# Kernel tuning notes

Measured on AMD Instinct MI355X. Metric: run time of the kernel, lower is better.

## Reference

```python
import jax, jax.numpy as jnp
import numpy as np
import math

B, L, IN, OUT = 32, 2048, 182, 2
H, N2, NL = 256, 32, 4  # hidden_dim, d_state//2, num_layers


def setup_inputs() -> dict:
    key = jax.random.key(0)
    ks = jax.random.split(key, 12)
    neural_input = jax.random.normal(ks[0], (B, L, IN), jnp.float32)
    # input / output projections
    Win = jax.random.normal(ks[1], (IN, H), jnp.float32) / np.sqrt(IN)
    b_in = jnp.zeros((H,), jnp.float32)
    Wout = jax.random.normal(ks[2], (H, OUT), jnp.float32) / np.sqrt(H)
    b_out = jnp.zeros((OUT,), jnp.float32)
    # stacked per-layer S4D params
    C2 = jax.random.normal(ks[3], (NL, H, N2, 2), jnp.float32)  # view_as_real of complex C
    log_dt = jax.random.uniform(ks[4], (NL, H), jnp.float32) * (math.log(0.1) - math.log(0.001)) + math.log(0.001)
    log_A_real = jnp.full((NL, H, N2), math.log(0.5), jnp.float32)
    A_imag = math.pi * jnp.broadcast_to(jnp.arange(N2, dtype=jnp.float32), (NL, H, N2))
    D = jax.random.normal(ks[5], (NL, H), jnp.float32)
    Wglu = jax.random.normal(ks[6], (NL, 2 * H, H), jnp.float32) / np.sqrt(H)
    bglu = jnp.zeros((NL, 2 * H), jnp.float32)
    return {"neural_input": neural_input, "Win": Win, "b_in": b_in,
            "C2": C2, "log_dt": log_dt, "log_A_real": log_A_real, "A_imag": A_imag,
            "D": D, "Wglu": Wglu, "bglu": bglu, "Wout": Wout, "b_out": b_out}


def _s4d_kernel(C2, log_dt, log_A_real, A_imag, length):
    # dt: (H,), A: (H,N2) complex
    dt = jnp.exp(log_dt)
    A = -jnp.exp(log_A_real) + 1j * A_imag
    dtA = A * dt[:, None]                      # (H, N2)
    C = (C2[..., 0] + 1j * C2[..., 1]) * (jnp.exp(dtA) - 1.0) / A
    t = jnp.arange(length, dtype=jnp.float32)
    E = jnp.exp(dtA[..., None] * t)            # (H, N2, L) complex
    K = 2.0 * jnp.einsum('hn,hnl->hl', C, E).real  # (H, L)
    return K


def _s4d_layer(u, C2, log_dt, log_A_real, A_imag, D, Wg, bg):
    # u: (B, H, L)
    length = u.shape[-1]
    k = _s4d_kernel(C2, log_dt, log_A_real, A_imag, length)
    k_f = jnp.fft.rfft(k, n=2 * length)        # (H, L+1)
    u_f = jnp.fft.rfft(u, n=2 * length)        # (B, H, L+1)
    y = jnp.fft.irfft(u_f * k_f, n=2 * length)[..., :length]
    y = y + u * D[:, None]
    y = jax.nn.gelu(y, approximate=False)      # nn.GELU default (erf)
    z = jnp.einsum('oh,bhl->bol', Wg, y) + bg[None, :, None]  # Conv1d k=1
    a, g = jnp.split(z, 2, axis=1)             # GLU over channel dim
    return a * jax.nn.sigmoid(g)


def reference(neural_input, Win, b_in, C2, log_dt, log_A_real, A_imag, D, Wglu, bglu, Wout, b_out):
    # input projection: (B, L, IN) -> (B, H, L)
    x = (neural_input @ Win + b_in).transpose(0, 2, 1)
    for i in range(NL):
        x = _s4d_layer(x, C2[i], log_dt[i], log_A_real[i], A_imag[i], D[i], Wglu[i], bglu[i])
    x = x.transpose(0, 2, 1)                   # (B, L, H)
    return x @ Wout + b_out                    # (B, L, OUT)
```

## Files before the change

### kernel.cpp

```cpp
#include <hip/hip_runtime.h>
#include <math.h>

typedef unsigned short u16;
typedef __attribute__((ext_vector_type(2))) unsigned short ushort2_t;
typedef __attribute__((ext_vector_type(4))) unsigned short ushort4_t;
typedef __attribute__((ext_vector_type(8))) unsigned short ushort8_t;
typedef __attribute__((ext_vector_type(8))) short short8;
typedef __attribute__((ext_vector_type(4))) float f32x4;

constexpr int Bn = 32, Ln = 2048, IN_DIM = 182, OUT_DIM = 2;
constexpr int Hn = 256, N2n = 32, NLn = 4;
constexpr int Tn = 64, NCn = Ln / Tn;
constexpr int KP = 192;

__device__ inline u16 f2bf(float f) {
  unsigned int u = __float_as_uint(f);
  u += 0x7fffu + ((u >> 16) & 1u);
  return (u16)(u >> 16);
}
__device__ inline float bf2f(u16 v) { return __uint_as_float(((unsigned int)v) << 16); }

__global__ void k_consts(const float* __restrict__ C2, const float* __restrict__ log_dt,
                         const float* __restrict__ log_A_real, const float* __restrict__ A_imag,
                         float* __restrict__ cAT, float* __restrict__ cC, float* __restrict__ cDt) {
  int idx = blockIdx.x * blockDim.x + threadIdx.x;
  if (idx >= NLn * Hn * N2n) return;
  int lh = idx / N2n;
  int h = lh % Hn;
  int l = lh / Hn;
  float dt = expf(log_dt[l * Hn + h]);
  float Ar = -expf(log_A_real[idx]);
  float Ai = A_imag[idx];
  float dr = Ar * dt, di = Ai * dt;
  float ea = expf(dr);
  float ar = ea * cosf(di), ai = ea * sinf(di);
  float eT = expf(dr * (float)Tn);
  cAT[idx * 2 + 0] = eT * cosf(di * (float)Tn);
  cAT[idx * 2 + 1] = eT * sinf(di * (float)Tn);
  float nr = ar - 1.0f, ni = ai;
  float inv = 1.0f / (Ar * Ar + Ai * Ai);
  float qr = (nr * Ar + ni * Ai) * inv;
  float qi = (ni * Ar - nr * Ai) * inv;
  float c2r = C2[idx * 2 + 0], c2i = C2[idx * 2 + 1];
  cC[idx * 2 + 0] = 2.0f * (c2r * qr - c2i * qi);
  cC[idx * 2 + 1] = 2.0f * (c2r * qi + c2i * qr);
  cDt[idx * 2 + 0] = dr;
  cDt[idx * 2 + 1] = di;
}

__global__ __launch_bounds__(256) void k_ktab(const float* __restrict__ cDt,
                                              const float* __restrict__ cC,
                                              float* __restrict__ ktab) {
  __shared__ float tmp[32][65];
  __shared__ float part[4][64];
  int lh = blockIdx.x;
  int tid = threadIdx.x;
  int n = tid >> 3, dq = tid & 7;
  float dr = cDt[(lh * N2n + n) * 2 + 0], di = cDt[(lh * N2n + n) * 2 + 1];
  float Cr = cC[(lh * N2n + n) * 2 + 0], Ci = cC[(lh * N2n + n) * 2 + 1];
  float d0 = (float)(dq * 8);
  float e0 = expf(dr * d0);
  float pr = e0 * cosf(di * d0), pi = e0 * sinf(di * d0);
  float ea = expf(dr);
  float ar = ea * cosf(di), ai = ea * sinf(di);
#pragma unroll
  for (int j = 0; j < 8; j++) {
    tmp[n][dq * 8 + j] = Cr * pr - Ci * pi;
    float t = pr * ar - pi * ai;
    pi = pr * ai + pi * ar;
    pr = t;
  }
  __syncthreads();
  int d = tid & 63, q = tid >> 6;
  float s = 0.0f;
#pragma unroll
  for (int k = 0; k < 8; k++) s += tmp[q * 8 + k][d];
  part[q][d] = s;
  __syncthreads();
  if (tid < 64) ktab[lh * 64 + tid] = part[0][tid] + part[1][tid] + part[2][tid] + part[3][tid];
}

__global__ void k_build(const float* __restrict__ cDt, const float* __restrict__ cC,
                        const float* __restrict__ ktab, const float* __restrict__ Dp,
                        u16* __restrict__ Lm, u16* __restrict__ Em, u16* __restrict__ Fm) {
  int h = blockIdx.x;
  int ym = blockIdx.y;
  int l = ym / 3, mat = ym % 3;
  int tid = threadIdx.x;
  int lh = l * Hn + h;
  if (mat == 2) {
    int n2 = tid & 31, tg = tid >> 5;
    float dr = cDt[(lh * N2n + n2) * 2 + 0], di = cDt[(lh * N2n + n2) * 2 + 1];
    float Cr = cC[(lh * N2n + n2) * 2 + 0], Ci = cC[(lh * N2n + n2) * 2 + 1];
    float p0 = (float)(tg * 8 + 1);
    float e0 = expf(dr * p0);
    float pr = e0 * cosf(di * p0), pi = e0 * sinf(di * p0);
    float ea = expf(dr);
    float ar = ea * cosf(di), ai = ea * sinf(di);
#pragma unroll
    for (int j = 0; j < 8; j++) {
      float wr = Cr * pr - Ci * pi;
      float wi = Cr * pi + Ci * pr;
      ushort2_t o; o[0] = f2bf(wr); o[1] = f2bf(-wi);
      *(ushort2_t*)(Fm + (size_t)lh * 4096 + (tg * 8 + j) * 64 + n2 * 2) = o;
      float t = pr * ar - pi * ai;
      pi = pr * ai + pi * ar;
      pr = t;
    }
    return;
  }
  int row = tid >> 2, tq = (tid & 3) * 16;
  u16 vals[16];
  if (mat == 0) {
    float Dh = Dp[lh];
    for (int j = 0; j < 16; j++) {
      int tau = tq + j;
      int d = row - tau;
      float v = 0.0f;
      if (d >= 0) { v = ktab[lh * 64 + d]; if (d == 0) v += Dh; }
      vals[j] = f2bf(v);
    }
  } else {
    int n = row >> 1, im = row & 1;
    float dr = cDt[(lh * N2n + n) * 2 + 0], di = cDt[(lh * N2n + n) * 2 + 1];
    float p0 = (float)(48 - tq);
    float e0 = expf(dr * p0);
    float pr = e0 * cosf(di * p0), pi = e0 * sinf(di * p0);
    float ea = expf(dr);
    float ar = ea * cosf(di), ai = ea * sinf(di);
#pragma unroll
    for (int j = 15; j >= 0; j--) {
      vals[j] = f2bf(im ? pi : pr);
      float t = pr * ar - pi * ai;
      pi = pr * ai + pi * ar;
      pr = t;
    }
  }
  u16* dst = (mat == 0 ? Lm : Em) + (size_t)lh * 4096 + row * 64 + tq;
  ushort8_t o0, o1;
  for (int j = 0; j < 8; j++) { o0[j] = vals[j]; o1[j] = vals[8 + j]; }
  *(ushort8_t*)dst = o0;
  *(ushort8_t*)(dst + 8) = o1;
}

__global__ void k_wf(const float* __restrict__ Wglu, u16* __restrict__ Wf) {
  int idx = blockIdx.x * blockDim.x + threadIdx.x;
  if (idx >= NLn * 2 * Hn * Hn) return;
  int k = idx & 255;
  int o = (idx >> 8) & 511;
  int l = idx >> 17;
  size_t off = (size_t)l * (32 * 8192) + (size_t)(o >> 4) * 8192
             + (size_t)(k >> 3) * 256 + (o & 15) * 16 + (k & 7) * 2;
  *(u16*)((char*)Wf + off) = f2bf(Wglu[idx]);
}

__global__ void k_wtin(const float* __restrict__ Win, u16* __restrict__ Wt) {
  int idx = blockIdx.x * blockDim.x + threadIdx.x;
  if (idx >= Hn * KP) return;
  int h = idx / KP, k = idx - h * KP;
  Wt[idx] = (k < IN_DIM) ? f2bf(Win[(size_t)k * Hn + h]) : (u16)0;
}

__global__ __launch_bounds__(256) void k_inproj(const float* __restrict__ nin,
                                                const u16* __restrict__ Wt,
                                                const float* __restrict__ b_in,
                                                u16* __restrict__ Xc) {
  int tid = threadIdx.x;
  int bx = blockIdx.x;
  int nb = blockIdx.y;
  int lane = tid & 63, wave = tid >> 6;
  int wm = wave >> 1, wn = wave & 1;
  int l15 = lane & 15, l4 = lane >> 4;
  int m0 = bx * 128 + wm * 64;
  int h0 = nb * 128 + wn * 64;
  f32x4 acc[4][4] = {};
#pragma unroll
  for (int ks = 0; ks < 6; ks++) {
    int k0 = ks * 32 + l4 * 8;
    short8 a[4], bfr[4];
#pragma unroll
    for (int mt = 0; mt < 4; mt++) {
      const float* rp = nin + (size_t)(m0 + mt * 16 + l15) * IN_DIM + k0;
      short8 v;
      if (k0 + 8 <= IN_DIM) {
        float2 f0 = *(const float2*)(rp);
        float2 f1 = *(const float2*)(rp + 2);
        float2 f2 = *(const float2*)(rp + 4);
        float2 f3 = *(const float2*)(rp + 6);
        v[0] = (short)f2bf(f0.x); v[1] = (short)f2bf(f0.y);
        v[2] = (short)f2bf(f1.x); v[3] = (short)f2bf(f1.y);
        v[4] = (short)f2bf(f2.x); v[5] = (short)f2bf(f2.y);
        v[6] = (short)f2bf(f3.x); v[7] = (short)f2bf(f3.y);
      } else {
#pragma unroll
        for (int j = 0; j < 8; j++) {
          int k = k0 + j;
          float x = (k < IN_DIM) ? rp[j] : 0.0f;
          v[j] = (short)f2bf(x);
        }
      }
      a[mt] = v;
    }
#pragma unroll
    for (int nt = 0; nt < 4; nt++)
      bfr[nt] = *(const short8*)(Wt + (size_t)(h0 + nt * 16 + l15) * KP + k0);
#pragma unroll
    for (int mt = 0; mt < 4; mt++)
#pragma unroll
      for (int nt = 0; nt < 4; nt++)
        acc[mt][nt] = __builtin_amdgcn_mfma_f32_16x16x32_bf16(a[mt], bfr[nt], acc[mt][nt], 0, 0, 0);
  }
#pragma unroll
  for (int mt = 0; mt < 4; mt++) {
#pragma unroll
    for (int nt = 0; nt < 4; nt++) {
      int j = h0 + nt * 16 + l15;
      float bb = b_in[j];
      int r0 = m0 + mt * 16 + l4 * 4;
      int b = r0 >> 11, li = r0 & 2047;
      int c = li >> 6, t0 = li & 63;
      ushort4_t w;
#pragma unroll
      for (int r = 0; r < 4; r++) w[r] = f2bf(acc[mt][nt][r] + bb);
      *(ushort4_t*)(Xc + ((size_t)(b * NCn + c) * Hn + j) * Tn + t0) = w;
    }
  }
}

__global__ __launch_bounds__(512, 6) void k_s4d(const u16* __restrict__ Xc,
                                                const u16* __restrict__ Lm,
                                                const u16* __restrict__ Em,
                                                const u16* __restrict__ Fm,
                                                const float* __restrict__ cAT,
                                                u16* __restrict__ Gf, int layer) {
  __shared__ __align__(16) char sbuf[32768];
  __shared__ __align__(16) char ybuf[16384];
  int tid = threadIdx.x;
  int lane = tid & 63, w = tid >> 6;
  int l15 = lane & 15, l4 = lane >> 4;
  int hg = blockIdx.x;
  int b = blockIdx.y;
  int h = hg * 8 + w;

  short8 ufr[2][2];
  const u16* xb = Xc + ((size_t)(b * NCn) * Hn + h) * Tn;
#pragma unroll
  for (int nt = 0; nt < 2; nt++)
#pragma unroll
    for (int ks = 0; ks < 2; ks++)
      ufr[nt][ks] = *(const short8*)(xb + (size_t)(nt * 16 + l15) * (Hn * Tn) + ks * 32 + l4 * 8);
  const u16* eb = Em + (size_t)(layer * Hn + h) * 4096;
#pragma unroll
  for (int mt = 0; mt < 4; mt++) {
    f32x4 sacc[2] = {};
#pragma unroll
    for (int ks = 0; ks < 2; ks++) {
      short8 af = *(const short8*)(eb + (mt * 16 + l15) * 64 + ks * 32 + l4 * 8);
#pragma unroll
      for (int nt = 0; nt < 2; nt++)
        sacc[nt] = __builtin_amdgcn_mfma_f32_16x16x32_bf16(af, ufr[nt][ks], sacc[nt], 0, 0, 0);
    }
    int comp0 = mt * 16 + l4 * 4;
    int g = comp0 >> 3, half = (comp0 >> 2) & 1;
#pragma unroll
    for (int nt = 0; nt < 2; nt++) {
      int c = nt * 16 + l15;
      ushort4_t wv;
#pragma unroll
      for (int r = 0; r < 4; r++) wv[r] = f2bf(sacc[nt][r]);
      *(ushort4_t*)(sbuf + w * 4096 + c * 128 + ((g ^ (c & 7)) << 4) + half * 8) = wv;
    }
  }
  __syncthreads();
  if (tid < 256) {
    int hl = tid >> 5, n = tid & 31;
    int hh = hg * 8 + hl;
    float aTr = cAT[((size_t)(layer * Hn + hh) * N2n + n) * 2 + 0];
    float aTi = cAT[((size_t)(layer * Hn + hh) * N2n + n) * 2 + 1];
    int grp = n >> 2, off = (n & 3) * 4;
    char* base = sbuf + hl * 4096;
    float cr = 0.0f, ci = 0.0f;
#pragma unroll
    for (int p = 0; p < 4; p++) {
      unsigned int sv[8];
#pragma unroll
      for (int q = 0; q < 8; q++) {
        int c = p * 8 + q;
        sv[q] = *(const unsigned int*)(base + c * 128 + ((grp ^ (c & 7)) << 4) + off);
      }
#pragma unroll
      for (int q = 0; q < 8; q++) {
        unsigned int s = sv[q];
        float sre = bf2f((u16)(s & 0xffffu));
        float sim = bf2f((u16)(s >> 16));
        sv[q] = (unsigned int)f2bf(cr) | ((unsigned int)f2bf(ci) << 16);
        float nr = aTr * cr - aTi * ci + sre;
        float ni = aTr * ci + aTi * cr + sim;
        cr = nr; ci = ni;
      }
#pragma unroll
      for (int q = 0; q < 8; q++) {
        int c = p * 8 + q;
        *(unsigned int*)(base + c * 128 + ((grp ^ (c & 7)) << 4) + off) = sv[q];
      }
    }
  }
  __syncthreads();
  const u16* lb = Lm + (size_t)(layer * Hn + h) * 4096;
  const u16* fb = Fm + (size_t)(layer * Hn + h) * 4096;
  u16* gp = Gf + (size_t)(hg * Bn + b) * Ln * 8;
  for (int nt = 0; nt < 2; nt++) {
    int c = nt * 16 + l15;
#pragma unroll
    for (int mt = 0; mt < 4; mt++) {
      f32x4 yacc = {};
#pragma unroll
      for (int ks = 0; ks < 2; ks++) {
        short8 af = *(const short8*)(lb + (mt * 16 + l15) * 64 + ks * 32 + l4 * 8);
        yacc = __builtin_amdgcn_mfma_f32_16x16x32_bf16(af, ufr[nt][ks], yacc, 0, 0, 0);
      }
#pragma unroll
      for (int ks = 0; ks < 2; ks++) {
        short8 af = *(const short8*)(fb + (mt * 16 + l15) * 64 + ks * 32 + l4 * 8);
        short8 bf = *(const short8*)(sbuf + w * 4096 + c * 128 + (((ks * 4 + l4) ^ (c & 7)) << 4));
        yacc = __builtin_amdgcn_mfma_f32_16x16x32_bf16(af, bf, yacc, 0, 0, 0);
      }
      int t0 = mt * 16 + l4 * 4;
      ushort4_t wv;
#pragma unroll
      for (int r = 0; r < 4; r++) {
        float y = yacc[r];
        wv[r] = f2bf(0.5f * y * (1.0f + erff(y * 0.70710678118654752f)));
      }
      int g = ((t0 >> 2) ^ l15) & 15;
      *(ushort4_t*)(ybuf + (l15 * 8 + w) * 128 + g * 8) = wv;
    }
    __syncthreads();
#pragma unroll
    for (int it = 0; it < 2; it++) {
      int mloc = it * 512 + tid;
      int cl = mloc >> 6, t = mloc & 63;
      int g = ((t >> 2) ^ cl) & 15;
      const char* bb = ybuf + (cl * 8) * 128 + g * 8 + (t & 3) * 2;
      ushort8_t o;
#pragma unroll
      for (int hl = 0; hl < 8; hl++) o[hl] = *(const u16*)(bb + hl * 128);
      int m = (nt * 16 + cl) * 64 + t;
      *(ushort8_t*)(gp + (size_t)m * 8) = o;
    }
    __syncthreads();
  }
}

template <int LAST>
__global__ __launch_bounds__(256) void k_glu(const u16* __restrict__ Gf,
                                             const u16* __restrict__ Wf,
                                             const float* __restrict__ bglu,
                                             u16* __restrict__ Xout, int layer) {
  int tid = threadIdx.x;
  int bx = blockIdx.x;
  int nb = blockIdx.y;
  int lane = tid & 63, wave = tid >> 6;
  int wm = wave >> 1, wn = wave & 1;
  int l15 = lane & 15, l4 = lane >> 4;
  int m0 = bx * 128 + wm * 64;
  const char* wb = (const char*)Wf + (size_t)layer * 262144 + lane * 16;
  f32x4 acc[4][4] = {};
#pragma unroll 2
  for (int ks = 0; ks < 8; ks++) {
    short8 a[4], bfr[4];
#pragma unroll
    for (int rg = 0; rg < 4; rg++)
      a[rg] = *(const short8*)(Gf + (size_t)(ks * 4 + l4) * 524288 + (size_t)(m0 + rg * 16 + l15) * 8);
#pragma unroll
    for (int ct = 0; ct < 2; ct++) {
      bfr[ct]     = *(const short8*)(wb + (size_t)(nb * 4 + wn * 2 + ct) * 8192 + ks * 1024);
      bfr[ct + 2] = *(const short8*)(wb + (size_t)(16 + nb * 4 + wn * 2 + ct) * 8192 + ks * 1024);
    }
#pragma unroll
    for (int rg = 0; rg < 4; rg++)
#pragma unroll
      for (int ct = 0; ct < 4; ct++)
        acc[rg][ct] = __builtin_amdgcn_mfma_f32_16x16x32_bf16(a[rg], bfr[ct], acc[rg][ct], 0, 0, 0);
  }
  int c0 = nb * 64 + wn * 32;
#pragma unroll
  for (int rg = 0; rg < 4; rg++) {
#pragma unroll
    for (int ct = 0; ct < 2; ct++) {
      int j = c0 + ct * 16 + l15;
      float ba = bglu[layer * 512 + j];
      float bg = bglu[layer * 512 + 256 + j];
      f32x4 va = acc[rg][ct], vg = acc[rg][ct + 2];
      int r0 = m0 + rg * 16 + l4 * 4;
      if (LAST) {
#pragma unroll
        for (int r = 0; r < 4; r++) {
          float za = va[r] + ba, zg = vg[r] + bg;
          Xout[(size_t)(r0 + r) * Hn + j] = f2bf(za / (1.0f + expf(-zg)));
        }
      } else {
        int b = r0 >> 11, li = r0 & 2047;
        int c = li >> 6, t0 = li & 63;
        ushort4_t w;
#pragma unroll
        for (int r = 0; r < 4; r++) {
          float za = va[r] + ba, zg = vg[r] + bg;
          w[r] = f2bf(za / (1.0f + expf(-zg)));
        }
        *(ushort4_t*)(Xout + ((size_t)(b * NCn + c) * Hn + j) * Tn + t0) = w;
      }
    }
  }
}

__global__ __launch_bounds__(256) void k_outproj(const u16* __restrict__ Xp,
                                                 const float* __restrict__ Wout,
                                                 const float* __restrict__ b_out,
                                                 float* __restrict__ out) {
  int row = blockIdx.x * 4 + (threadIdx.x >> 6);
  int lane = threadIdx.x & 63;
  ushort4_t xv = *(const ushort4_t*)(Xp + (size_t)row * Hn + lane * 4);
  float x0 = bf2f(xv[0]), x1 = bf2f(xv[1]), x2 = bf2f(xv[2]), x3 = bf2f(xv[3]);
  const float4 w01 = *(const float4*)&Wout[lane * 8];
  const float4 w23 = *(const float4*)&Wout[lane * 8 + 4];
  float p0 = x0 * w01.x + x1 * w01.z + x2 * w23.x + x3 * w23.z;
  float p1 = x0 * w01.y + x1 * w01.w + x2 * w23.y + x3 * w23.w;
  for (int off = 32; off; off >>= 1) {
    p0 += __shfl_down(p0, off, 64);
    p1 += __shfl_down(p1, off, 64);
  }
  if (lane == 0) {
    out[(size_t)row * 2 + 0] = p0 + b_out[0];
    out[(size_t)row * 2 + 1] = p1 + b_out[1];
  }
}

extern "C" void kernel_launch(void* const* d_in, const int* in_sizes, int n_in,
                              void* d_out, int out_size, void* d_ws, size_t ws_size,
                              hipStream_t stream) {
  const float* nin        = (const float*)d_in[0];
  const float* Win        = (const float*)d_in[1];
  const float* b_in       = (const float*)d_in[2];
  const float* C2         = (const float*)d_in[3];
  const float* log_dt     = (const float*)d_in[4];
  const float* log_A_real = (const float*)d_in[5];
  const float* A_imag     = (const float*)d_in[6];
  const float* Dp         = (const float*)d_in[7];
  const float* Wglu       = (const float*)d_in[8];
  const float* bglu       = (const float*)d_in[9];
  const float* Wout       = (const float*)d_in[10];
  const float* b_out      = (const float*)d_in[11];
  float* out = (float*)d_out;

  u16* Xc = (u16*)d_ws;
  u16* Gf = Xc + (size_t)16777216;
  u16* Wt = Gf + (size_t)16777216;
  u16* Wf = Wt + (size_t)49152;
  u16* Lm = Wf + (size_t)524288;
  u16* Em = Lm + (size_t)4194304;
  u16* Fm = Em + (size_t)4194304;
  float* ktab = (float*)(Fm + (size_t)4194304);
  float* cAT  = ktab + 65536;
  float* cC   = cAT + 65536;
  float* cDt  = cC + 65536;

  k_consts<<<(NLn * Hn * N2n + 255) / 256, 256, 0, stream>>>(C2, log_dt, log_A_real, A_imag, cAT, cC, cDt);
  k_ktab<<<NLn * Hn, 256, 0, stream>>>(cDt, cC, ktab);
  k_build<<<dim3(Hn, NLn * 3), 256, 0, stream>>>(cDt, cC, ktab, Dp, Lm, Em, Fm);
  k_wf<<<(NLn * 2 * Hn * Hn + 255) / 256, 256, 0, stream>>>(Wglu, Wf);
  k_wtin<<<(Hn * KP + 255) / 256, 256, 0, stream>>>(Win, Wt);
  k_inproj<<<dim3(512, 2), 256, 0, stream>>>(nin, Wt, b_in, Xc);
  for (int l = 0; l < NLn; l++) {
    k_s4d<<<dim3(32, Bn), 512, 0, stream>>>(Xc, Lm, Em, Fm, cAT, Gf, l);
    if (l < NLn - 1)
      k_glu<0><<<dim3(512, 4), 256, 0, stream>>>(Gf, Wf, bglu, Xc, l);
    else
      k_glu<1><<<dim3(512, 4), 256, 0, stream>>>(Gf, Wf, bglu, Xc, l);
  }
  k_outproj<<<Bn * Ln / 4, 256, 0, stream>>>(Xc, Wout, b_out, out);
}
```

Before: 518.4 us.

## Fuse S4D prep kernels, stage input tile in LDS, remap block order

Three setup kernels (consts, ktab, build) are merged into one per-(layer,h) kernel that holds the intermediate constants in shared memory, which removes two launches and the global round-trips for ktab/cC/cDt. The input projection now loads its 128-row fp32 tile coalesced into padded LDS as bf16 before the MFMA loop, instead of doing strided per-lane float2 loads. The s4d and glu launches switch to 1D grids with a swizzled block-to-tile mapping so that consecutive blocks are spread across the XCDs, meant to improve cache locality. The inproj kernel uses about 51KB of LDS, which may lower its occupancy.

```diff
diff --git a/kernel.cpp b/kernel.cpp
--- a/kernel.cpp
+++ b/kernel.cpp
@@ -12,6 +12,7 @@
 constexpr int Hn = 256, N2n = 32, NLn = 4;
 constexpr int Tn = 64, NCn = Ln / Tn;
 constexpr int KP = 192;
+constexpr int IPPAD = 200;
 
 __device__ inline u16 f2bf(float f) {
   unsigned int u = __float_as_uint(f);
@@ -20,78 +21,111 @@
 }
 __device__ inline float bf2f(u16 v) { return __uint_as_float(((unsigned int)v) << 16); }
 
-__global__ void k_consts(const float* __restrict__ C2, const float* __restrict__ log_dt,
-                         const float* __restrict__ log_A_real, const float* __restrict__ A_imag,
-                         float* __restrict__ cAT, float* __restrict__ cC, float* __restrict__ cDt) {
-  int idx = blockIdx.x * blockDim.x + threadIdx.x;
-  if (idx >= NLn * Hn * N2n) return;
-  int lh = idx / N2n;
-  int h = lh % Hn;
-  int l = lh / Hn;
-  float dt = expf(log_dt[l * Hn + h]);
-  float Ar = -expf(log_A_real[idx]);
-  float Ai = A_imag[idx];
-  float dr = Ar * dt, di = Ai * dt;
-  float ea = expf(dr);
-  float ar = ea * cosf(di), ai = ea * sinf(di);
-  float eT = expf(dr * (float)Tn);
-  cAT[idx * 2 + 0] = eT * cosf(di * (float)Tn);
-  cAT[idx * 2 + 1] = eT * sinf(di * (float)Tn);
-  float nr = ar - 1.0f, ni = ai;
-  float inv = 1.0f / (Ar * Ar + Ai * Ai);
-  float qr = (nr * Ar + ni * Ai) * inv;
-  float qi = (ni * Ar - nr * Ai) * inv;
-  float c2r = C2[idx * 2 + 0], c2i = C2[idx * 2 + 1];
-  cC[idx * 2 + 0] = 2.0f * (c2r * qr - c2i * qi);
-  cC[idx * 2 + 1] = 2.0f * (c2r * qi + c2i * qr);
-  cDt[idx * 2 + 0] = dr;
-  cDt[idx * 2 + 1] = di;
-}
-
-__global__ __launch_bounds__(256) void k_ktab(const float* __restrict__ cDt,
-                                              const float* __restrict__ cC,
-                                              float* __restrict__ ktab) {
+__global__ __launch_bounds__(256) void k_prep(const float* __restrict__ C2,
+                                              const float* __restrict__ log_dt,
+                                              const float* __restrict__ log_A_real,
+                                              const float* __restrict__ A_imag,
+                                              const float* __restrict__ Dp,
+                                              float* __restrict__ cAT,
+                                              u16* __restrict__ Lm, u16* __restrict__ Em,
+                                              u16* __restrict__ Fm) {
+  __shared__ float sdr[32], sdi[32], sCr[32], sCi[32];
   __shared__ float tmp[32][65];
   __shared__ float part[4][64];
+  __shared__ float kt[64];
   int lh = blockIdx.x;
   int tid = threadIdx.x;
-  int n = tid >> 3, dq = tid & 7;
-  float dr = cDt[(lh * N2n + n) * 2 + 0], di = cDt[(lh * N2n + n) * 2 + 1];
-  float Cr = cC[(lh * N2n + n) * 2 + 0], Ci = cC[(lh * N2n + n) * 2 + 1];
-  float d0 = (float)(dq * 8);
-  float e0 = expf(dr * d0);
-  float pr = e0 * cosf(di * d0), pi = e0 * sinf(di * d0);
-  float ea = expf(dr);
-  float ar = ea * cosf(di), ai = ea * sinf(di);
-#pragma unroll
-  for (int j = 0; j < 8; j++) {
-    tmp[n][dq * 8 + j] = Cr * pr - Ci * pi;
-    float t = pr * ar - pi * ai;
-    pi = pr * ai + pi * ar;
-    pr = t;
-  }
-  __syncthreads();
-  int d = tid & 63, q = tid >> 6;
-  float s = 0.0f;
-#pragma unroll
-  for (int k = 0; k < 8; k++) s += tmp[q * 8 + k][d];
-  part[q][d] = s;
-  __syncthreads();
-  if (tid < 64) ktab[lh * 64 + tid] = part[0][tid] + part[1][tid] + part[2][tid] + part[3][tid];
-}
-
-__global__ void k_build(const float* __restrict__ cDt, const float* __restrict__ cC,
-                        const float* __restrict__ ktab, const float* __restrict__ Dp,
-                        u16* __restrict__ Lm, u16* __restrict__ Em, u16* __restrict__ Fm) {
-  int h = blockIdx.x;
-  int ym = blockIdx.y;
-  int l = ym / 3, mat = ym % 3;
-  int tid = threadIdx.x;
-  int lh = l * Hn + h;
-  if (mat == 2) {
+  if (tid < 32) {
+    int n = tid;
+    int idx = lh * N2n + n;
+    float dt = expf(log_dt[lh]);
+    float Ar = -expf(log_A_real[idx]);
+    float Ai = A_imag[idx];
+    float dr = Ar * dt, di = Ai * dt;
+    float ea = expf(dr);
+    float ar = ea * cosf(di), ai = ea * sinf(di);
+    float eT = expf(dr * 64.0f);
+    cAT[idx * 2 + 0] = eT * cosf(di * 64.0f);
+    cAT[idx * 2 + 1] = eT * sinf(di * 64.0f);
+    float nr = ar - 1.0f, ni = ai;
+    float inv = 1.0f / (Ar * Ar + Ai * Ai);
+    float qr = (nr * Ar + ni * Ai) * inv;
+    float qi = (ni * Ar - nr * Ai) * inv;
+    float c2r = C2[idx * 2 + 0], c2i = C2[idx * 2 + 1];
+    sdr[n] = dr; sdi[n] = di;
+    sCr[n] = 2.0f * (c2r * qr - c2i * qi);
+    sCi[n] = 2.0f * (c2r * qi + c2i * qr);
+  }
+  __syncthreads();
+  {
+    int n = tid >> 3, dq = tid & 7;
+    float dr = sdr[n], di = sdi[n], Cr = sCr[n], Ci = sCi[n];
+    float d0 = (float)(dq * 8);
+    float e0 = expf(dr * d0);
+    float pr = e0 * cosf(di * d0), pi = e0 * sinf(di * d0);
+    float ea = expf(dr);
+    float ar = ea * cosf(di), ai = ea * sinf(di);
+#pragma unroll
+    for (int j = 0; j < 8; j++) {
+      tmp[n][dq * 8 + j] = Cr * pr - Ci * pi;
+      float t = pr * ar - pi * ai;
+      pi = pr * ai + pi * ar;
+      pr = t;
+    }
+  }
+  __syncthreads();
+  {
+    int d = tid & 63, q = tid >> 6;
+    float s = 0.0f;
+#pragma unroll
+    for (int k = 0; k < 8; k++) s += tmp[q * 8 + k][d];
+    part[q][d] = s;
+  }
+  __syncthreads();
+  if (tid < 64) kt[tid] = part[0][tid] + part[1][tid] + part[2][tid] + part[3][tid];
+  __syncthreads();
+  {
+    int row = tid >> 2, tq = (tid & 3) * 16;
+    float Dh = Dp[lh];
+    u16 vals[16];
+    for (int j = 0; j < 16; j++) {
+      int d = row - (tq + j);
+      float v = 0.0f;
+      if (d >= 0) { v = kt[d]; if (d == 0) v += Dh; }
+      vals[j] = f2bf(v);
+    }
+    u16* dst = Lm + (size_t)lh * 4096 + row * 64 + tq;
+    ushort8_t o0, o1;
+    for (int j = 0; j < 8; j++) { o0[j] = vals[j]; o1[j] = vals[8 + j]; }
+    *(ushort8_t*)dst = o0;
+    *(ushort8_t*)(dst + 8) = o1;
+  }
+  {
+    int row = tid >> 2, tq = (tid & 3) * 16;
+    int n = row >> 1, im = row & 1;
+    float dr = sdr[n], di = sdi[n];
+    float p0 = (float)(48 - tq);
+    float e0 = expf(dr * p0);
+    float pr = e0 * cosf(di * p0), pi = e0 * sinf(di * p0);
+    float ea = expf(dr);
+    float ar = ea * cosf(di), ai = ea * sinf(di);
+    u16 vals[16];
+#pragma unroll
+    for (int j = 15; j >= 0; j--) {
+      vals[j] = f2bf(im ? pi : pr);
+      float t = pr * ar - pi * ai;
+      pi = pr * ai + pi * ar;
+      pr = t;
+    }
+    u16* dst = Em + (size_t)lh * 4096 + row * 64 + tq;
+    ushort8_t o0, o1;
+    for (int j = 0; j < 8; j++) { o0[j] = vals[j]; o1[j] = vals[8 + j]; }
+    *(ushort8_t*)dst = o0;
+    *(ushort8_t*)(dst + 8) = o1;
+  }
+  {
     int n2 = tid & 31, tg = tid >> 5;
-    float dr = cDt[(lh * N2n + n2) * 2 + 0], di = cDt[(lh * N2n + n2) * 2 + 1];
-    float Cr = cC[(lh * N2n + n2) * 2 + 0], Ci = cC[(lh * N2n + n2) * 2 + 1];
+    float dr = sdr[n2], di = sdi[n2], Cr = sCr[n2], Ci = sCi[n2];
     float p0 = (float)(tg * 8 + 1);
     float e0 = expf(dr * p0);
     float pr = e0 * cosf(di * p0), pi = e0 * sinf(di * p0);
@@ -107,40 +141,7 @@
       pi = pr * ai + pi * ar;
       pr = t;
     }
-    return;
-  }
-  int row = tid >> 2, tq = (tid & 3) * 16;
-  u16 vals[16];
-  if (mat == 0) {
-    float Dh = Dp[lh];
-    for (int j = 0; j < 16; j++) {
-      int tau = tq + j;
-      int d = row - tau;
-      float v = 0.0f;
-      if (d >= 0) { v = ktab[lh * 64 + d]; if (d == 0) v += Dh; }
-      vals[j] = f2bf(v);
-    }
-  } else {
-    int n = row >> 1, im = row & 1;
-    float dr = cDt[(lh * N2n + n) * 2 + 0], di = cDt[(lh * N2n + n) * 2 + 1];
-    float p0 = (float)(48 - tq);
-    float e0 = expf(dr * p0);
-    float pr = e0 * cosf(di * p0), pi = e0 * sinf(di * p0);
-    float ea = expf(dr);
-    float ar = ea * cosf(di), ai = ea * sinf(di);
-#pragma unroll
-    for (int j = 15; j >= 0; j--) {
-      vals[j] = f2bf(im ? pi : pr);
-      float t = pr * ar - pi * ai;
-      pi = pr * ai + pi * ar;
-      pr = t;
-    }
-  }
-  u16* dst = (mat == 0 ? Lm : Em) + (size_t)lh * 4096 + row * 64 + tq;
-  ushort8_t o0, o1;
-  for (int j = 0; j < 8; j++) { o0[j] = vals[j]; o1[j] = vals[8 + j]; }
-  *(ushort8_t*)dst = o0;
-  *(ushort8_t*)(dst + 8) = o1;
+  }
 }
 
 __global__ void k_wf(const float* __restrict__ Wglu, u16* __restrict__ Wf) {
@@ -165,13 +166,33 @@
                                                 const u16* __restrict__ Wt,
                                                 const float* __restrict__ b_in,
                                                 u16* __restrict__ Xc) {
+  __shared__ __align__(16) u16 at[128 * IPPAD];
   int tid = threadIdx.x;
   int bx = blockIdx.x;
   int nb = blockIdx.y;
+  int m0 = bx * 128;
+  for (int i = tid; i < 128 * (IPPAD - IN_DIM); i += 256) {
+    int r = i / (IPPAD - IN_DIM), c = IN_DIM + i - r * (IPPAD - IN_DIM);
+    at[r * IPPAD + c] = 0;
+  }
+  const float4* src = (const float4*)(nin + (size_t)m0 * IN_DIM);
+  for (int i = tid; i < 128 * IN_DIM / 4; i += 256) {
+    float4 v = src[i];
+    int e0 = i * 4;
+    int r = e0 / IN_DIM;
+    int c = e0 - r * IN_DIM;
+    float vv[4] = {v.x, v.y, v.z, v.w};
+#pragma unroll
+    for (int j = 0; j < 4; j++) {
+      int rr = r, cc = c + j;
+      if (cc >= IN_DIM) { rr++; cc -= IN_DIM; }
+      at[rr * IPPAD + cc] = f2bf(vv[j]);
+    }
+  }
+  __syncthreads();
   int lane = tid & 63, wave = tid >> 6;
   int wm = wave >> 1, wn = wave & 1;
   int l15 = lane & 15, l4 = lane >> 4;
-  int m0 = bx * 128 + wm * 64;
   int h0 = nb * 128 + wn * 64;
   f32x4 acc[4][4] = {};
 #pragma unroll
@@ -179,28 +200,8 @@
     int k0 = ks * 32 + l4 * 8;
     short8 a[4], bfr[4];
 #pragma unroll
-    for (int mt = 0; mt < 4; mt++) {
-      const float* rp = nin + (size_t)(m0 + mt * 16 + l15) * IN_DIM + k0;
-      short8 v;
-      if (k0 + 8 <= IN_DIM) {
-        float2 f0 = *(const float2*)(rp);
-        float2 f1 = *(const float2*)(rp + 2);
-        float2 f2 = *(const float2*)(rp + 4);
-        float2 f3 = *(const float2*)(rp + 6);
-        v[0] = (short)f2bf(f0.x); v[1] = (short)f2bf(f0.y);
-        v[2] = (short)f2bf(f1.x); v[3] = (short)f2bf(f1.y);
-        v[4] = (short)f2bf(f2.x); v[5] = (short)f2bf(f2.y);
-        v[6] = (short)f2bf(f3.x); v[7] = (short)f2bf(f3.y);
-      } else {
-#pragma unroll
-        for (int j = 0; j < 8; j++) {
-          int k = k0 + j;
-          float x = (k < IN_DIM) ? rp[j] : 0.0f;
-          v[j] = (short)f2bf(x);
-        }
-      }
-      a[mt] = v;
-    }
+    for (int mt = 0; mt < 4; mt++)
+      a[mt] = *(const short8*)&at[(wm * 64 + mt * 16 + l15) * IPPAD + k0];
 #pragma unroll
     for (int nt = 0; nt < 4; nt++)
       bfr[nt] = *(const short8*)(Wt + (size_t)(h0 + nt * 16 + l15) * KP + k0);
@@ -216,7 +217,7 @@
     for (int nt = 0; nt < 4; nt++) {
       int j = h0 + nt * 16 + l15;
       float bb = b_in[j];
-      int r0 = m0 + mt * 16 + l4 * 4;
+      int r0 = m0 + wm * 64 + mt * 16 + l4 * 4;
       int b = r0 >> 11, li = r0 & 2047;
       int c = li >> 6, t0 = li & 63;
       ushort4_t w;
@@ -238,8 +239,10 @@
   int tid = threadIdx.x;
   int lane = tid & 63, w = tid >> 6;
   int l15 = lane & 15, l4 = lane >> 4;
-  int hg = blockIdx.x;
-  int b = blockIdx.y;
+  int flat = blockIdx.x;
+  int vid = (flat & 7) * 128 + (flat >> 3);
+  int hg = vid >> 5;
+  int b = vid & 31;
   int h = hg * 8 + w;
 
   short8 ufr[2][2];
@@ -358,8 +361,10 @@
                                              const float* __restrict__ bglu,
                                              u16* __restrict__ Xout, int layer) {
   int tid = threadIdx.x;
-  int bx = blockIdx.x;
-  int nb = blockIdx.y;
+  int flat = blockIdx.x;
+  int vid = (flat & 7) * 256 + (flat >> 3);
+  int bx = vid >> 2;
+  int nb = vid & 3;
   int lane = tid & 63, wave = tid >> 6;
   int wm = wave >> 1, wn = wave & 1;
   int l15 = lane & 15, l4 = lane >> 4;
@@ -460,23 +465,18 @@
   u16* Lm = Wf + (size_t)524288;
   u16* Em = Lm + (size_t)4194304;
   u16* Fm = Em + (size_t)4194304;
-  float* ktab = (float*)(Fm + (size_t)4194304);
-  float* cAT  = ktab + 65536;
-  float* cC   = cAT + 65536;
-  float* cDt  = cC + 65536;
-
-  k_consts<<<(NLn * Hn * N2n + 255) / 256, 256, 0, stream>>>(C2, log_dt, log_A_real, A_imag, cAT, cC, cDt);
-  k_ktab<<<NLn * Hn, 256, 0, stream>>>(cDt, cC, ktab);
-  k_build<<<dim3(Hn, NLn * 3), 256, 0, stream>>>(cDt, cC, ktab, Dp, Lm, Em, Fm);
+  float* cAT = (float*)(Fm + (size_t)4194304);
+
+  k_prep<<<NLn * Hn, 256, 0, stream>>>(C2, log_dt, log_A_real, A_imag, Dp, cAT, Lm, Em, Fm);
   k_wf<<<(NLn * 2 * Hn * Hn + 255) / 256, 256, 0, stream>>>(Wglu, Wf);
   k_wtin<<<(Hn * KP + 255) / 256, 256, 0, stream>>>(Win, Wt);
   k_inproj<<<dim3(512, 2), 256, 0, stream>>>(nin, Wt, b_in, Xc);
   for (int l = 0; l < NLn; l++) {
-    k_s4d<<<dim3(32, Bn), 512, 0, stream>>>(Xc, Lm, Em, Fm, cAT, Gf, l);
+    k_s4d<<<1024, 512, 0, stream>>>(Xc, Lm, Em, Fm, cAT, Gf, l);
     if (l < NLn - 1)
-      k_glu<0><<<dim3(512, 4), 256, 0, stream>>>(Gf, Wf, bglu, Xc, l);
+      k_glu<0><<<2048, 256, 0, stream>>>(Gf, Wf, bglu, Xc, l);
     else
-      k_glu<1><<<dim3(512, 4), 256, 0, stream>>>(Gf, Wf, bglu, Xc, l);
+      k_glu<1><<<2048, 256, 0, stream>>>(Gf, Wf, bglu, Xc, l);
   }
   k_outproj<<<Bn * Ln / 4, 256, 0, stream>>>(Xc, Wout, b_out, out);
 }
```

New measurement: 496.5 us. 4.2% less time.
